# Kernel optimization log

Hardware: AMD Instinct MI355X
Metric: run time of the kernel (lower is better)

## Reference

```python
import jax, jax.numpy as jnp
import numpy as np

E, D_IN, D_H, D_OUT = 8, 1024, 4096, 1024
N_TOK = 4096


def setup_inputs() -> dict:
    key = jax.random.key(0)
    ks = jax.random.split(key, 7)
    s1 = 1.0 / np.sqrt(D_IN)
    s2 = 1.0 / np.sqrt(D_H)
    return {
        "x": jax.random.normal(ks[0], (N_TOK, D_IN), dtype=jnp.float32),
        "W1": jax.random.uniform(ks[1], (E, D_IN, D_H), jnp.float32, -s1, s1),
        "b1": jax.random.uniform(ks[2], (E, D_H), jnp.float32, -s1, s1),
        "W2": jax.random.uniform(ks[3], (E, D_H, D_OUT), jnp.float32, -s2, s2),
        "b2": jax.random.uniform(ks[4], (E, D_OUT), jnp.float32, -s2, s2),
        "Wg": jax.random.uniform(ks[5], (D_IN, E), jnp.float32, -s1, s1),
        "bg": jax.random.uniform(ks[6], (E,), jnp.float32, -s1, s1),
    }


def reference(x, W1, b1, W2, b2, Wg, bg):
    # gate: [N, E] softmax over experts
    gate = jax.nn.softmax(x @ Wg + bg, axis=-1)
    # all-experts 2-layer MLP, batched over experts
    h = jax.nn.relu(jnp.einsum('ni,eih->neh', x, W1) + b1)          # [N, E, H]
    y = jnp.einsum('neh,eho->neo', h, W2) + b2                      # [N, E, O]
    # gate-weighted sum over experts
    return jnp.einsum('ne,neo->no', gate, y)                        # [N, O]
```

## Files before the change

kernel.cpp:

```cpp
#include <hip/hip_runtime.h>

#define E_EXP 8
#define D_IN 1024
#define D_H 4096
#define D_OUT 1024
#define N_TOK 4096

using f32x4  = __attribute__((ext_vector_type(4))) float;
using bf16x8 = __attribute__((ext_vector_type(8))) __bf16;

typedef __attribute__((address_space(1))) void gvoid_t;
typedef __attribute__((address_space(3))) void lvoid_t;

__device__ __forceinline__ void async_load16(const void* g, void* l) {
    __builtin_amdgcn_global_load_lds((gvoid_t*)g, (lvoid_t*)l, 16, 0, 0);
}

__device__ __forceinline__ unsigned short f2bf(float f) {
    unsigned int x = __float_as_uint(f);
    x += 0x7fffu + ((x >> 16) & 1u);
    return (unsigned short)(x >> 16);
}

__global__ __launch_bounds__(256) void cast_x_kernel(const float* __restrict__ in,
                                                     unsigned short* __restrict__ outp) {
    int i = blockIdx.x * 256 + threadIdx.x;
    float4 f = ((const float4*)in)[i];
    ushort4 u;
    u.x = f2bf(f.x); u.y = f2bf(f.y); u.z = f2bf(f.z); u.w = f2bf(f.w);
    ((ushort4*)outp)[i] = u;
}

__global__ __launch_bounds__(256) void gate_kernel(const float* __restrict__ x,
                                                   const float* __restrict__ Wg,
                                                   const float* __restrict__ bg,
                                                   float* __restrict__ gate) {
    int wave = threadIdx.x >> 6, lane = threadIdx.x & 63;
    int n = blockIdx.x * 4 + wave;
    int e = lane & 7, part = lane >> 3;
    const float* xr = x + (size_t)n * D_IN + part * (D_IN / 8);
    const float* wr = Wg + (size_t)part * (D_IN / 8) * E_EXP + e;
    float s = 0.f;
#pragma unroll 4
    for (int d = 0; d < D_IN / 8; d++) s += xr[d] * wr[d * E_EXP];
    s += __shfl_xor(s, 8);
    s += __shfl_xor(s, 16);
    s += __shfl_xor(s, 32);
    s += bg[e];
    float m = s;
    m = fmaxf(m, __shfl_xor(m, 1));
    m = fmaxf(m, __shfl_xor(m, 2));
    m = fmaxf(m, __shfl_xor(m, 4));
    float ex = __expf(s - m);
    float sum = ex;
    sum += __shfl_xor(sum, 1);
    sum += __shfl_xor(sum, 2);
    sum += __shfl_xor(sum, 4);
    if (lane < 8) gate[n * 8 + lane] = ex / sum;
}

__global__ __launch_bounds__(256) void transpose_cast(const float* __restrict__ in,
                                                      unsigned short* __restrict__ outp,
                                                      int R, int C) {
    in   += (size_t)blockIdx.z * R * C;
    outp += (size_t)blockIdx.z * R * C;
    __shared__ float tile[32][33];
    int x = threadIdx.x & 31, y = threadIdx.x >> 5;
    int r0 = blockIdx.y * 32, c0 = blockIdx.x * 32;
#pragma unroll
    for (int i = 0; i < 32; i += 8)
        tile[y + i][x] = in[(size_t)(r0 + y + i) * C + c0 + x];
    __syncthreads();
#pragma unroll
    for (int i = 0; i < 32; i += 8) {
        int c = y + i;
        outp[(size_t)(c0 + c) * R + r0 + x] = f2bf(tile[x][c]);
    }
}

__global__ __launch_bounds__(256) void out_init_kernel(const float* __restrict__ gate,
                                                       const float* __restrict__ b2,
                                                       float* __restrict__ out) {
    int i = blockIdx.x * 256 + threadIdx.x;
    int n = i / (D_OUT / 4), o4 = i % (D_OUT / 4);
    const float* g = gate + n * 8;
    float4 s = make_float4(0.f, 0.f, 0.f, 0.f);
#pragma unroll
    for (int e = 0; e < E_EXP; e++) {
        float4 b = ((const float4*)(b2 + (size_t)e * D_OUT))[o4];
        float ge = g[e];
        s.x += ge * b.x; s.y += ge * b.y; s.z += ge * b.z; s.w += ge * b.w;
    }
    ((float4*)out)[i] = s;
}

template <int MODE>
__global__ __launch_bounds__(256) void gemm_kernel(const unsigned short* __restrict__ Abase,
                                                   const unsigned short* __restrict__ Wbase,
                                                   const float* __restrict__ b1a,
                                                   const float* __restrict__ gate,
                                                   unsigned short* __restrict__ Hout,
                                                   float* __restrict__ out,
                                                   int e0, size_t hstride) {
    __shared__ __align__(16) unsigned short As[128 * 64];
    __shared__ __align__(16) unsigned short Bs[128 * 64];
    const int t = threadIdx.x;
    const int wave = t >> 6;
    const int lane = t & 63;
    const int quad = lane >> 4;
    const int l16 = lane & 15;

    const int lin = blockIdx.x;
    const int xcd = lin & 7;
    const int s = lin >> 3;
    int n_t, er, m_t;
    if (MODE == 0) {
        n_t = s & 31;
        int em = s >> 5;
        er = em >> 2;
        m_t = (em & 3) + xcd * 4;
    } else {
        n_t = s & 7;
        int em = s >> 3;
        er = em >> 2;
        m_t = (em & 3) + xcd * 4;
    }
    const int e = e0 + er;
    const int n0 = n_t * 128;
    const int m0 = m_t * 128;
    const int ld = (MODE == 0) ? D_IN : D_H;
    const int K  = (MODE == 0) ? D_IN : D_H;

    const unsigned short* A = Abase + (MODE == 1 ? (size_t)er * hstride : (size_t)0);
    const unsigned short* B = Wbase + (size_t)e * 4194304;

    const int r0 = t >> 3;
    const int gk = ((t & 7) ^ (r0 & 7)) << 3;
    const unsigned short* aP = A + (size_t)(m0 + r0) * ld + gk;
    const unsigned short* bP = B + (size_t)(n0 + r0) * ld + gk;

    const int wm = (wave & 1) * 64;
    const int wn = (wave >> 1) * 64;
    f32x4 acc[4][4] = {};

    for (int k = 0; k < K; k += 64) {
#pragma unroll
        for (int j = 0; j < 4; j++)
            async_load16(aP + k + (size_t)j * 32 * ld, &As[(j * 256 + wave * 64) * 8]);
#pragma unroll
        for (int j = 0; j < 4; j++)
            async_load16(bP + k + (size_t)j * 32 * ld, &Bs[(j * 256 + wave * 64) * 8]);
        __syncthreads();
#pragma unroll
        for (int half = 0; half < 2; half++) {
            bf16x8 af[4], bfr[4];
#pragma unroll
            for (int i = 0; i < 4; i++) {
                int row = wm + i * 16 + l16;
                af[i] = *reinterpret_cast<const bf16x8*>(
                    &As[row * 64 + (((half << 2) + quad) ^ (row & 7)) * 8]);
            }
#pragma unroll
            for (int j = 0; j < 4; j++) {
                int row = wn + j * 16 + l16;
                bfr[j] = *reinterpret_cast<const bf16x8*>(
                    &Bs[row * 64 + (((half << 2) + quad) ^ (row & 7)) * 8]);
            }
#pragma unroll
            for (int i = 0; i < 4; i++)
#pragma unroll
                for (int j = 0; j < 4; j++)
                    acc[i][j] = __builtin_amdgcn_mfma_f32_16x16x32_bf16(af[i], bfr[j], acc[i][j], 0, 0, 0);
        }
        __syncthreads();
    }

    const int mrow = m0 + wm + quad * 4;
    const int ncol = n0 + wn + l16;
    if (MODE == 0) {
        const float* bias = b1a + (size_t)e * D_H;
        unsigned short* Hbase = Hout + (size_t)er * hstride;
#pragma unroll
        for (int i = 0; i < 4; i++) {
#pragma unroll
            for (int r = 0; r < 4; r++) {
                int row = mrow + i * 16 + r;
                float g = gate[row * 8 + e];
                unsigned short* hr = Hbase + (size_t)row * D_H;
#pragma unroll
                for (int j = 0; j < 4; j++) {
                    int col = ncol + j * 16;
                    float v = fmaxf(acc[i][j][r] + bias[col], 0.f) * g;
                    hr[col] = f2bf(v);
                }
            }
        }
    } else {
#pragma unroll
        for (int i = 0; i < 4; i++) {
#pragma unroll
            for (int r = 0; r < 4; r++) {
                int row = mrow + i * 16 + r;
                float* orow = out + (size_t)row * D_OUT;
#pragma unroll
                for (int j = 0; j < 4; j++) {
                    int col = ncol + j * 16;
                    unsafeAtomicAdd(&orow[col], acc[i][j][r]);
                }
            }
        }
    }
}

extern "C" void kernel_launch(void* const* d_in, const int* in_sizes, int n_in,
                              void* d_out, int out_size, void* d_ws, size_t ws_size,
                              hipStream_t stream) {
    const float* x  = (const float*)d_in[0];
    const float* W1 = (const float*)d_in[1];
    const float* b1 = (const float*)d_in[2];
    const float* W2 = (const float*)d_in[3];
    const float* b2 = (const float*)d_in[4];
    const float* Wg = (const float*)d_in[5];
    const float* bg = (const float*)d_in[6];
    float* out = (float*)d_out;

    char* p = (char*)d_ws;
    unsigned short* xb  = (unsigned short*)p; p += (size_t)N_TOK * D_IN * 2;
    unsigned short* W1T = (unsigned short*)p; p += (size_t)E_EXP * D_IN * D_H * 2;
    unsigned short* W2T = (unsigned short*)p; p += (size_t)E_EXP * D_H * D_OUT * 2;
    float* gate         = (float*)p;          p += (size_t)N_TOK * E_EXP * 4;
    unsigned short* h   = (unsigned short*)p;

    const size_t hstride = (size_t)N_TOK * D_H;

    cast_x_kernel<<<dim3(N_TOK * D_IN / 1024), 256, 0, stream>>>(x, xb);
    gate_kernel<<<dim3(N_TOK / 4), 256, 0, stream>>>(x, Wg, bg, gate);
    transpose_cast<<<dim3(D_H / 32, D_IN / 32, E_EXP), 256, 0, stream>>>(W1, W1T, D_IN, D_H);
    transpose_cast<<<dim3(D_OUT / 32, D_H / 32, E_EXP), 256, 0, stream>>>(W2, W2T, D_H, D_OUT);
    out_init_kernel<<<dim3(N_TOK * D_OUT / 1024), 256, 0, stream>>>(gate, b2, out);

    for (int g = 0; g < 2; g++) {
        gemm_kernel<0><<<dim3(4096), 256, 0, stream>>>(
            xb, W1T, b1, gate, h, nullptr, g * 4, hstride);
        gemm_kernel<1><<<dim3(1024), 256, 0, stream>>>(
            h, W2T, nullptr, nullptr, nullptr, out, g * 4, hstride);
    }
}
```

Measured before the change: 1.119 ms.

## Enlarge GEMM tiles to 256x128 and vectorize cast and transpose kernels

The GEMM block tile grows from 128x128 to 256x128. Each wave now computes 128x64 with 8x4 MFMA accumulators, which raises arithmetic intensity and halves the number of blocks. The transpose-cast kernel moves to 64x64 tiles with float4 loads and 8-wide bf16 stores, and the x cast now processes 8 elements per thread. The larger tile raises register and LDS pressure, which could hurt occupancy, and a 512-block second GEMM may leave some compute units underfilled.

```diff
diff --git a/kernel.cpp b/kernel.cpp
--- a/kernel.cpp
+++ b/kernel.cpp
@@ -8,6 +8,7 @@
 
 using f32x4  = __attribute__((ext_vector_type(4))) float;
 using bf16x8 = __attribute__((ext_vector_type(8))) __bf16;
+using us8    = __attribute__((ext_vector_type(8))) unsigned short;
 
 typedef __attribute__((address_space(1))) void gvoid_t;
 typedef __attribute__((address_space(3))) void lvoid_t;
@@ -25,10 +26,12 @@
 __global__ __launch_bounds__(256) void cast_x_kernel(const float* __restrict__ in,
                                                      unsigned short* __restrict__ outp) {
     int i = blockIdx.x * 256 + threadIdx.x;
-    float4 f = ((const float4*)in)[i];
-    ushort4 u;
-    u.x = f2bf(f.x); u.y = f2bf(f.y); u.z = f2bf(f.z); u.w = f2bf(f.w);
-    ((ushort4*)outp)[i] = u;
+    float4 f0 = ((const float4*)in)[i * 2];
+    float4 f1 = ((const float4*)in)[i * 2 + 1];
+    us8 u;
+    u[0] = f2bf(f0.x); u[1] = f2bf(f0.y); u[2] = f2bf(f0.z); u[3] = f2bf(f0.w);
+    u[4] = f2bf(f1.x); u[5] = f2bf(f1.y); u[6] = f2bf(f1.z); u[7] = f2bf(f1.w);
+    ((us8*)outp)[i] = u;
 }
 
 __global__ __launch_bounds__(256) void gate_kernel(const float* __restrict__ x,
@@ -59,22 +62,36 @@
     if (lane < 8) gate[n * 8 + lane] = ex / sum;
 }
 
-__global__ __launch_bounds__(256) void transpose_cast(const float* __restrict__ in,
-                                                      unsigned short* __restrict__ outp,
-                                                      int R, int C) {
+__global__ __launch_bounds__(256) void transpose_cast64(const float* __restrict__ in,
+                                                        unsigned short* __restrict__ outp,
+                                                        int R, int C) {
     in   += (size_t)blockIdx.z * R * C;
     outp += (size_t)blockIdx.z * R * C;
-    __shared__ float tile[32][33];
-    int x = threadIdx.x & 31, y = threadIdx.x >> 5;
-    int r0 = blockIdx.y * 32, c0 = blockIdx.x * 32;
-#pragma unroll
-    for (int i = 0; i < 32; i += 8)
-        tile[y + i][x] = in[(size_t)(r0 + y + i) * C + c0 + x];
+    __shared__ float tile[64][65];
+    const int t = threadIdx.x;
+    const int r0 = blockIdx.y * 64, c0 = blockIdx.x * 64;
+    {
+        int r = t >> 4, cc = (t & 15) * 4;
+#pragma unroll
+        for (int p = 0; p < 4; p++) {
+            float4 v = *(const float4*)(in + (size_t)(r0 + p * 16 + r) * C + c0 + cc);
+            tile[p * 16 + r][cc]     = v.x;
+            tile[p * 16 + r][cc + 1] = v.y;
+            tile[p * 16 + r][cc + 2] = v.z;
+            tile[p * 16 + r][cc + 3] = v.w;
+        }
+    }
     __syncthreads();
-#pragma unroll
-    for (int i = 0; i < 32; i += 8) {
-        int c = y + i;
-        outp[(size_t)(c0 + c) * R + r0 + x] = f2bf(tile[x][c]);
+    {
+        int c = t >> 3, w = t & 7;
+#pragma unroll
+        for (int p = 0; p < 2; p++) {
+            int cc = p * 32 + c;
+            us8 v;
+#pragma unroll
+            for (int i = 0; i < 8; i++) v[i] = f2bf(tile[w * 8 + i][cc]);
+            *(us8*)(outp + (size_t)(c0 + cc) * R + r0 + w * 8) = v;
+        }
     }
 }
 
@@ -95,14 +112,14 @@
 }
 
 template <int MODE>
-__global__ __launch_bounds__(256) void gemm_kernel(const unsigned short* __restrict__ Abase,
-                                                   const unsigned short* __restrict__ Wbase,
-                                                   const float* __restrict__ b1a,
-                                                   const float* __restrict__ gate,
-                                                   unsigned short* __restrict__ Hout,
-                                                   float* __restrict__ out,
-                                                   int e0, size_t hstride) {
-    __shared__ __align__(16) unsigned short As[128 * 64];
+__global__ __launch_bounds__(256, 2) void gemm_kernel(const unsigned short* __restrict__ Abase,
+                                                      const unsigned short* __restrict__ Wbase,
+                                                      const float* __restrict__ b1a,
+                                                      const float* __restrict__ gate,
+                                                      unsigned short* __restrict__ Hout,
+                                                      float* __restrict__ out,
+                                                      int e0, size_t hstride) {
+    __shared__ __align__(16) unsigned short As[256 * 64];
     __shared__ __align__(16) unsigned short Bs[128 * 64];
     const int t = threadIdx.x;
     const int wave = t >> 6;
@@ -117,17 +134,17 @@
     if (MODE == 0) {
         n_t = s & 31;
         int em = s >> 5;
-        er = em >> 2;
-        m_t = (em & 3) + xcd * 4;
+        er = em >> 1;
+        m_t = (em & 1) + xcd * 2;
     } else {
         n_t = s & 7;
         int em = s >> 3;
-        er = em >> 2;
-        m_t = (em & 3) + xcd * 4;
+        er = em >> 1;
+        m_t = (em & 1) + xcd * 2;
     }
     const int e = e0 + er;
     const int n0 = n_t * 128;
-    const int m0 = m_t * 128;
+    const int m0 = m_t * 256;
     const int ld = (MODE == 0) ? D_IN : D_H;
     const int K  = (MODE == 0) ? D_IN : D_H;
 
@@ -139,13 +156,13 @@
     const unsigned short* aP = A + (size_t)(m0 + r0) * ld + gk;
     const unsigned short* bP = B + (size_t)(n0 + r0) * ld + gk;
 
-    const int wm = (wave & 1) * 64;
+    const int wm = (wave & 1) * 128;
     const int wn = (wave >> 1) * 64;
-    f32x4 acc[4][4] = {};
+    f32x4 acc[8][4] = {};
 
     for (int k = 0; k < K; k += 64) {
 #pragma unroll
-        for (int j = 0; j < 4; j++)
+        for (int j = 0; j < 8; j++)
             async_load16(aP + k + (size_t)j * 32 * ld, &As[(j * 256 + wave * 64) * 8]);
 #pragma unroll
         for (int j = 0; j < 4; j++)
@@ -153,9 +170,9 @@
         __syncthreads();
 #pragma unroll
         for (int half = 0; half < 2; half++) {
-            bf16x8 af[4], bfr[4];
-#pragma unroll
-            for (int i = 0; i < 4; i++) {
+            bf16x8 af[8], bfr[4];
+#pragma unroll
+            for (int i = 0; i < 8; i++) {
                 int row = wm + i * 16 + l16;
                 af[i] = *reinterpret_cast<const bf16x8*>(
                     &As[row * 64 + (((half << 2) + quad) ^ (row & 7)) * 8]);
@@ -167,7 +184,7 @@
                     &Bs[row * 64 + (((half << 2) + quad) ^ (row & 7)) * 8]);
             }
 #pragma unroll
-            for (int i = 0; i < 4; i++)
+            for (int i = 0; i < 8; i++)
 #pragma unroll
                 for (int j = 0; j < 4; j++)
                     acc[i][j] = __builtin_amdgcn_mfma_f32_16x16x32_bf16(af[i], bfr[j], acc[i][j], 0, 0, 0);
@@ -181,7 +198,7 @@
         const float* bias = b1a + (size_t)e * D_H;
         unsigned short* Hbase = Hout + (size_t)er * hstride;
 #pragma unroll
-        for (int i = 0; i < 4; i++) {
+        for (int i = 0; i < 8; i++) {
 #pragma unroll
             for (int r = 0; r < 4; r++) {
                 int row = mrow + i * 16 + r;
@@ -197,7 +214,7 @@
         }
     } else {
 #pragma unroll
-        for (int i = 0; i < 4; i++) {
+        for (int i = 0; i < 8; i++) {
 #pragma unroll
             for (int r = 0; r < 4; r++) {
                 int row = mrow + i * 16 + r;
@@ -233,16 +250,16 @@
 
     const size_t hstride = (size_t)N_TOK * D_H;
 
-    cast_x_kernel<<<dim3(N_TOK * D_IN / 1024), 256, 0, stream>>>(x, xb);
+    cast_x_kernel<<<dim3(N_TOK * D_IN / 2048), 256, 0, stream>>>(x, xb);
     gate_kernel<<<dim3(N_TOK / 4), 256, 0, stream>>>(x, Wg, bg, gate);
-    transpose_cast<<<dim3(D_H / 32, D_IN / 32, E_EXP), 256, 0, stream>>>(W1, W1T, D_IN, D_H);
-    transpose_cast<<<dim3(D_OUT / 32, D_H / 32, E_EXP), 256, 0, stream>>>(W2, W2T, D_H, D_OUT);
+    transpose_cast64<<<dim3(D_H / 64, D_IN / 64, E_EXP), 256, 0, stream>>>(W1, W1T, D_IN, D_H);
+    transpose_cast64<<<dim3(D_OUT / 64, D_H / 64, E_EXP), 256, 0, stream>>>(W2, W2T, D_H, D_OUT);
     out_init_kernel<<<dim3(N_TOK * D_OUT / 1024), 256, 0, stream>>>(gate, b2, out);
 
     for (int g = 0; g < 2; g++) {
-        gemm_kernel<0><<<dim3(4096), 256, 0, stream>>>(
+        gemm_kernel<0><<<dim3(2048), 256, 0, stream>>>(
             xb, W1T, b1, gate, h, nullptr, g * 4, hstride);
-        gemm_kernel<1><<<dim3(1024), 256, 0, stream>>>(
+        gemm_kernel<1><<<dim3(512), 256, 0, stream>>>(
             h, W2T, nullptr, nullptr, nullptr, out, g * 4, hstride);
     }
 }
```

Result: faster. 935.0 us (-16.4%).
